# Optimization experiments

Measured on AMD Instinct MI355X. Metric: run time of the kernel, lower is better.

The kernel has to match this reference:

```python
import jax, jax.numpy as jnp
import numpy as np

B, C, CI, H, W = 4, 128, 64, 64, 64


def conv1x1(x, w, b):
    # x: [B,C,H,W], w: [Cout,Cin], b: [Cout]
    return jnp.einsum('bchw,oc->bohw', x, w) + b[None, :, None, None]


def setup_inputs() -> dict:
    key = jax.random.key(0)
    ks = jax.random.split(key, 10)
    s = 0.05  # keep logits in a sane range for softmax
    return {
        'x0': jax.random.normal(ks[0], (B, C, H, W), jnp.float32),
        'x1': jax.random.normal(ks[1], (B, C, H, W), jnp.float32),
        'g_w': jax.random.normal(ks[2], (CI, C), jnp.float32) * s,
        'g_b': jax.random.normal(ks[3], (CI,), jnp.float32) * s,
        'theta_w': jax.random.normal(ks[4], (CI, C), jnp.float32) * s,
        'theta_b': jax.random.normal(ks[5], (CI,), jnp.float32) * s,
        'phi_w': jax.random.normal(ks[6], (CI, C), jnp.float32) * s,
        'phi_b': jax.random.normal(ks[7], (CI,), jnp.float32) * s,
        'W_w': jax.random.normal(ks[8], (C, CI), jnp.float32) * s,
        'W_b': jax.random.normal(ks[9], (C,), jnp.float32) * s,
    }


def reference(x0, x1, g_w, g_b, theta_w, theta_b, phi_w, phi_b, W_w, W_b):
    b, c, h, w = x0.shape
    n = h * w
    ci = g_w.shape[0]
    g_x = conv1x1(x0, g_w, g_b).reshape(b, ci, n).transpose(0, 2, 1)      # [B,N,Ci]
    theta_x = conv1x1(x1, theta_w, theta_b).reshape(b, ci, n).transpose(0, 2, 1)  # [B,N,Ci]
    phi_x = conv1x1(x0, phi_w, phi_b).reshape(b, ci, n)                    # [B,Ci,N]
    f = jnp.einsum('bqc,bck->bqk', theta_x, phi_x)                         # [B,N,N]
    f_div_C = jax.nn.softmax(f, axis=-1)
    y = jnp.einsum('bqk,bkc->bqc', f_div_C, g_x)                           # [B,N,Ci]
    y = y.transpose(0, 2, 1).reshape(b, ci, h, w)
    W_y = conv1x1(y, W_w, W_b)
    return W_y + x0
```

## Files before the change

kernel.cpp:

```cpp
#include <hip/hip_runtime.h>
#include <hip/hip_bf16.h>


typedef unsigned int   u32;
typedef unsigned short u16;
typedef __attribute__((ext_vector_type(8))) short short8;
typedef __attribute__((ext_vector_type(4))) short short4v;
typedef __attribute__((ext_vector_type(4))) float f32x4;

#define LOG2E 1.4426950408889634f
#define KSPLIT 8

__device__ __forceinline__ float b2f(u16 v) {
  union { u32 u; float f; } x; x.u = ((u32)v) << 16; return x.f;
}
__device__ __forceinline__ u16 f2b(float f) {
  u32 u = __float_as_uint(f);
  return (u16)((u + 0x8000u) >> 16);
}
__device__ __forceinline__ short8 load_w_frag(const float* p, float s) {
  const float4 f0 = ((const float4*)p)[0];
  const float4 f1 = ((const float4*)p)[1];
  union { u32 w[4]; short8 s8; } r;
  r.w[0] = (u32)f2b(f0.x * s) | ((u32)f2b(f0.y * s) << 16);
  r.w[1] = (u32)f2b(f0.z * s) | ((u32)f2b(f0.w * s) << 16);
  r.w[2] = (u32)f2b(f1.x * s) | ((u32)f2b(f1.y * s) << 16);
  r.w[3] = (u32)f2b(f1.z * s) | ((u32)f2b(f1.w * s) << 16);
  return r.s8;
}


__global__ __launch_bounds__(256) void qkv_fused_kernel(
    const float* __restrict__ x0, const float* __restrict__ x1,
    const float* __restrict__ tw, const float* __restrict__ tb,
    const float* __restrict__ pw, const float* __restrict__ pb,
    const float* __restrict__ gw, const float* __restrict__ gb,
    u16* __restrict__ Q, u16* __restrict__ K, u16* __restrict__ Vt)
{
  const int n0 = blockIdx.x * 64;
  const int b  = blockIdx.y;
  const int t  = threadIdx.x;

  __shared__ __align__(16) short xt[2][64][136];

  #pragma unroll 8
  for (int i = 0; i < 64; ++i) {
    const int idx = i * 256 + t;
    const int tensor = idx >> 13;
    const int c = (idx >> 6) & 127;
    const int n = idx & 63;
    const float v = (tensor ? x1 : x0)[((size_t)b * 128 + c) * 4096 + n0 + n];
    xt[tensor][n][c] = (short)f2b(v);
  }
  asm volatile("" ::: "memory");
  __syncthreads();

  const int wave = t >> 6;
  const int lane = t & 63;
  const int quad = lane >> 4, l15 = lane & 15;

  if (wave < 2) {
    const int conv = wave;
    const float* wsrc = conv ? pw : tw;
    const float  ws   = conv ? 1.f : LOG2E;
    const short* xl   = &xt[conv ? 0 : 1][0][0];

    f32x4 acc[4][4];
    #pragma unroll
    for (int i = 0; i < 4; ++i)
      #pragma unroll
      for (int j = 0; j < 4; ++j) acc[i][j] = (f32x4){0.f, 0.f, 0.f, 0.f};

    #pragma unroll
    for (int kk = 0; kk < 4; ++kk) {
      short8 wf[4], xf[4];
      #pragma unroll
      for (int ot = 0; ot < 4; ++ot)
        wf[ot] = load_w_frag(wsrc + (ot * 16 + l15) * 128 + kk * 32 + quad * 8, ws);
      #pragma unroll
      for (int nt = 0; nt < 4; ++nt)
        xf[nt] = *(const short8*)(xl + (nt * 16 + l15) * 136 + kk * 32 + quad * 8);
      #pragma unroll
      for (int i = 0; i < 4; ++i)
        #pragma unroll
        for (int j = 0; j < 4; ++j)
          acc[i][j] = __builtin_amdgcn_mfma_f32_16x16x32_bf16(xf[i], wf[j], acc[i][j], 0, 0, 0);
    }

    u16* dst = (conv ? K : Q) + (size_t)b * 4096 * 64;
    const float* bias = conv ? pb : tb;
    const float bscale = conv ? 1.f : LOG2E;
    #pragma unroll
    for (int ot = 0; ot < 4; ++ot) {
      const float bv = bias[ot * 16 + l15] * bscale;
      #pragma unroll
      for (int nt = 0; nt < 4; ++nt)
        #pragma unroll
        for (int r = 0; r < 4; ++r) {
          const int n = n0 + nt * 16 + quad * 4 + r;
          dst[(size_t)n * 64 + ot * 16 + l15] = f2b(acc[nt][ot][r] + bv);
        }
    }
  } else {
    const int oh = wave - 2;
    const short* xl = &xt[0][0][0];

    f32x4 acc[2][4];
    #pragma unroll
    for (int i = 0; i < 2; ++i)
      #pragma unroll
      for (int j = 0; j < 4; ++j) acc[i][j] = (f32x4){0.f, 0.f, 0.f, 0.f};

    #pragma unroll
    for (int kk = 0; kk < 4; ++kk) {
      short8 wf[2], xf[4];
      #pragma unroll
      for (int ot = 0; ot < 2; ++ot)
        wf[ot] = load_w_frag(gw + ((oh * 2 + ot) * 16 + l15) * 128 + kk * 32 + quad * 8, 1.f);
      #pragma unroll
      for (int nt = 0; nt < 4; ++nt)
        xf[nt] = *(const short8*)(xl + (nt * 16 + l15) * 136 + kk * 32 + quad * 8);
      #pragma unroll
      for (int i = 0; i < 2; ++i)
        #pragma unroll
        for (int j = 0; j < 4; ++j)
          acc[i][j] = __builtin_amdgcn_mfma_f32_16x16x32_bf16(wf[i], xf[j], acc[i][j], 0, 0, 0);
    }

    u16* dst = Vt + (size_t)b * 64 * 4096;
    #pragma unroll
    for (int ot = 0; ot < 2; ++ot)
      #pragma unroll
      for (int r = 0; r < 4; ++r) {
        const int o = (oh * 2 + ot) * 16 + quad * 4 + r;
        const float bv = gb[o];
        #pragma unroll
        for (int nc = 0; nc < 4; ++nc)
          dst[(size_t)o * 4096 + n0 + nc * 16 + l15] = f2b(acc[ot][nc][r] + bv);
      }
  }
}

__global__ __launch_bounds__(256) void attn_kernel(
    const u16* __restrict__ Q, const u16* __restrict__ K,
    const u16* __restrict__ Vt, u16* __restrict__ Opart,
    float* __restrict__ Lp)
{
  const int qt = blockIdx.x, b = blockIdx.y, ks = blockIdx.z;
  const int tid  = threadIdx.x;
  const int wave = tid >> 6;
  const int lane = tid & 63;
  const int quad = lane >> 4;
  const int l15  = lane & 15;

  __shared__ __align__(16) short P_lds[4][64][72];
  short* pw = &P_lds[wave][0][0];

  const int q0 = qt * 256 + wave * 64;
  const u16* Qb = Q  + (size_t)b * 4096 * 64;
  const u16* Kb = K  + (size_t)b * 4096 * 64;
  const u16* Vb = Vt + (size_t)b * 64 * 4096;

  short8 qf[4][2];
  #pragma unroll
  for (int nt = 0; nt < 4; ++nt) {
    const u16* qp = Qb + (size_t)(q0 + nt * 16 + l15) * 64 + quad * 8;
    qf[nt][0] = *(const short8*)qp;
    qf[nt][1] = *(const short8*)(qp + 32);
  }

  f32x4 oacc[4][4];
  #pragma unroll
  for (int i = 0; i < 4; ++i)
    #pragma unroll
    for (int j = 0; j < 4; ++j)
      oacc[i][j] = (f32x4){0.f, 0.f, 0.f, 0.f};
  float lsum[4] = {0.f, 0.f, 0.f, 0.f};

  const int kbase = ks * (4096 / KSPLIT);
  const int NKT   = 4096 / KSPLIT / 64;

  short8 kf[4][2];
  #pragma unroll
  for (int mt = 0; mt < 4; ++mt) {
    const u16* kp = Kb + (size_t)(kbase + mt * 16 + l15) * 64 + quad * 8;
    kf[mt][0] = *(const short8*)kp;
    kf[mt][1] = *(const short8*)(kp + 32);
  }

  for (int kt = 0; kt < NKT; ++kt) {
    const int k0 = kbase + kt * 64;

    short8 vf[4][2];
    #pragma unroll
    for (int nd = 0; nd < 4; ++nd) {
      const u16* vp = Vb + (size_t)(nd * 16 + l15) * 4096 + k0 + quad * 8;
      vf[nd][0] = *(const short8*)vp;
      vf[nd][1] = *(const short8*)(vp + 32);
    }

    #pragma unroll
    for (int mt = 0; mt < 4; ++mt) {
      #pragma unroll
      for (int nt = 0; nt < 4; ++nt) {
        f32x4 s = {0.f, 0.f, 0.f, 0.f};
        s = __builtin_amdgcn_mfma_f32_16x16x32_bf16(kf[mt][0], qf[nt][0], s, 0, 0, 0);
        s = __builtin_amdgcn_mfma_f32_16x16x32_bf16(kf[mt][1], qf[nt][1], s, 0, 0, 0);
        float p0 = exp2f(s[0]), p1 = exp2f(s[1]), p2 = exp2f(s[2]), p3 = exp2f(s[3]);
        lsum[nt] += (p0 + p1) + (p2 + p3);
        u32 u0 = __float_as_uint(p0) + 0x8000u;
        u32 u1 = __float_as_uint(p1) + 0x8000u;
        u32 u2 = __float_as_uint(p2) + 0x8000u;
        u32 u3 = __float_as_uint(p3) + 0x8000u;
        union { uint2 u; short4v s4; } pk;
        pk.u.x = __builtin_amdgcn_perm(u1, u0, 0x07060302u);
        pk.u.y = __builtin_amdgcn_perm(u3, u2, 0x07060302u);
        *(short4v*)(pw + (nt * 16 + l15) * 72 + mt * 16 + quad * 4) = pk.s4;
      }
    }

    if (kt < NKT - 1) {
      #pragma unroll
      for (int mt = 0; mt < 4; ++mt) {
        const u16* kp = Kb + (size_t)(k0 + 64 + mt * 16 + l15) * 64 + quad * 8;
        kf[mt][0] = *(const short8*)kp;
        kf[mt][1] = *(const short8*)(kp + 32);
      }
    }

    asm volatile("" ::: "memory");

    #pragma unroll
    for (int mq = 0; mq < 4; ++mq) {
      const short* pr = pw + (mq * 16 + l15) * 72 + quad * 8;
      short8 pa0 = *(const short8*)pr;
      short8 pa1 = *(const short8*)(pr + 32);
      #pragma unroll
      for (int nd = 0; nd < 4; ++nd) {
        oacc[mq][nd] = __builtin_amdgcn_mfma_f32_16x16x32_bf16(pa0, vf[nd][0], oacc[mq][nd], 0, 0, 0);
        oacc[mq][nd] = __builtin_amdgcn_mfma_f32_16x16x32_bf16(pa1, vf[nd][1], oacc[mq][nd], 0, 0, 0);
      }
    }

    asm volatile("" ::: "memory");
  }

  #pragma unroll
  for (int nt = 0; nt < 4; ++nt) {
    float v = lsum[nt];
    v += __shfl_xor(v, 16, 64);
    v += __shfl_xor(v, 32, 64);
    lsum[nt] = v;
  }
  float* LpB = Lp + ((size_t)ks * 4 + b) * 4096;
  if (quad == 0) {
    #pragma unroll
    for (int nt = 0; nt < 4; ++nt)
      LpB[q0 + nt * 16 + l15] = lsum[nt];
  }

  u16* Ob = Opart + ((size_t)ks * 4 + b) * 4096 * 64;
  #pragma unroll
  for (int mq = 0; mq < 4; ++mq)
    #pragma unroll
    for (int nd = 0; nd < 4; ++nd)
      #pragma unroll
      for (int r = 0; r < 4; ++r) {
        int q = q0 + mq * 16 + quad * 4 + r;
        Ob[(size_t)q * 64 + nd * 16 + l15] = f2b(oacc[mq][nd][r]);
      }
}

__global__ __launch_bounds__(256) void out_fused_kernel(
    const u16* __restrict__ Opart, const float* __restrict__ Lp,
    const float* __restrict__ Wf, const float* __restrict__ Wbf,
    const float* __restrict__ x0, float* __restrict__ out)
{
  const int n0 = blockIdx.x * 64;
  const int b  = blockIdx.y;
  const int t  = threadIdx.x;

  __shared__ __align__(16) short Ys[64][72];

  {
    const int nl = t >> 2;
    const int q4 = t & 3;
    const int ng = n0 + nl;

    float l = 0.f;
    #pragma unroll
    for (int ks = 0; ks < KSPLIT; ++ks)
      l += Lp[((size_t)ks * 4 + b) * 4096 + ng];

    float a[16];
    #pragma unroll
    for (int j = 0; j < 16; ++j) a[j] = 0.f;
    #pragma unroll
    for (int ks = 0; ks < KSPLIT; ++ks) {
      const uint4* row = (const uint4*)(Opart + (((size_t)ks * 4 + b) * 4096 + ng) * 64 + q4 * 16);
      #pragma unroll
      for (int v = 0; v < 2; ++v) {
        uint4 r = row[v];
        u32 wds[4] = {r.x, r.y, r.z, r.w};
        #pragma unroll
        for (int j = 0; j < 4; ++j) {
          a[v * 8 + 2 * j]     += __uint_as_float(wds[j] << 16);
          a[v * 8 + 2 * j + 1] += __uint_as_float(wds[j] & 0xffff0000u);
        }
      }
    }
    const float rinv = 1.f / l;
    union { u32 w[8]; short8 s8[2]; } pk;
    #pragma unroll
    for (int j = 0; j < 8; ++j)
      pk.w[j] = (u32)f2b(a[2 * j] * rinv) | ((u32)f2b(a[2 * j + 1] * rinv) << 16);
    *(short8*)&Ys[nl][q4 * 16]     = pk.s8[0];
    *(short8*)&Ys[nl][q4 * 16 + 8] = pk.s8[1];
  }
  asm volatile("" ::: "memory");
  __syncthreads();

  const int wave = t >> 6;
  const int lane = t & 63;
  const int quad = lane >> 4, l15 = lane & 15;

  f32x4 acc[2][4];
  #pragma unroll
  for (int i = 0; i < 2; ++i)
    #pragma unroll
    for (int j = 0; j < 4; ++j) acc[i][j] = (f32x4){0.f, 0.f, 0.f, 0.f};

  #pragma unroll
  for (int kk = 0; kk < 2; ++kk) {
    short8 wf[2], yf[4];
    #pragma unroll
    for (int ot = 0; ot < 2; ++ot)
      wf[ot] = load_w_frag(Wf + ((wave * 2 + ot) * 16 + l15) * 64 + kk * 32 + quad * 8, 1.f);
    #pragma unroll
    for (int nt = 0; nt < 4; ++nt)
      yf[nt] = *(const short8*)&Ys[nt * 16 + l15][kk * 32 + quad * 8];
    #pragma unroll
    for (int i = 0; i < 2; ++i)
      #pragma unroll
      for (int j = 0; j < 4; ++j)
        acc[i][j] = __builtin_amdgcn_mfma_f32_16x16x32_bf16(wf[i], yf[j], acc[i][j], 0, 0, 0);
  }

  #pragma unroll
  for (int ot = 0; ot < 2; ++ot)
    #pragma unroll
    for (int r = 0; r < 4; ++r) {
      const int o = (wave * 2 + ot) * 16 + quad * 4 + r;
      const float bv = Wbf[o];
      #pragma unroll
      for (int nt = 0; nt < 4; ++nt) {
        const size_t idx = ((size_t)(b * 128 + o)) * 4096 + n0 + nt * 16 + l15;
        out[idx] = acc[ot][nt][r] + bv + x0[idx];
      }
    }
}

extern "C" void kernel_launch(void* const* d_in, const int* in_sizes, int n_in,
                              void* d_out, int out_size, void* d_ws, size_t ws_size,
                              hipStream_t stream) {
  const float* x0 = (const float*)d_in[0];
  const float* x1 = (const float*)d_in[1];
  const float* gw = (const float*)d_in[2];
  const float* gb = (const float*)d_in[3];
  const float* tw = (const float*)d_in[4];
  const float* tb = (const float*)d_in[5];
  const float* pw = (const float*)d_in[6];
  const float* pb = (const float*)d_in[7];
  const float* Ww = (const float*)d_in[8];
  const float* Wb = (const float*)d_in[9];
  float* out = (float*)d_out;

  char* ws = (char*)d_ws;
  u16*   Qw    = (u16*)(ws + 0);
  u16*   Kw    = (u16*)(ws + (2u << 20));
  u16*   Vtw   = (u16*)(ws + (4u << 20));
  u16*   Opart = (u16*)(ws + (6u << 20));
  float* Lp    = (float*)(ws + (22u << 20));

  qkv_fused_kernel<<<dim3(64, 4), dim3(256), 0, stream>>>(
      x0, x1, tw, tb, pw, pb, gw, gb, Qw, Kw, Vtw);

  attn_kernel<<<dim3(16, 4, KSPLIT), dim3(256), 0, stream>>>(Qw, Kw, Vtw, Opart, Lp);

  out_fused_kernel<<<dim3(64, 4), dim3(256), 0, stream>>>(
      Opart, Lp, Ww, Wb, x0, out);
}
```

Before: 137.3 us.

## Stage K/V tiles in double-buffered LDS shared across waves; vectorize input transpose

The attention kernel now loads each 64-key K tile and V tile once per block into double-buffered shared memory with coalesced 16-byte loads, prefetching the next tile into registers while the current one is computed. Previously each of the four waves fetched the same K/V fragments from global memory on its own. This cuts redundant global/L2 traffic by up to 4x, at the cost of extra LDS, two block-wide barriers per iteration, and possibly lower occupancy. The QKV kernel's input transpose also switches to float4 loads with scattered 2-byte LDS stores.

Result: faster. 133.5 us (-2.8%).

```diff
diff --git a/kernel.cpp b/kernel.cpp
--- a/kernel.cpp
+++ b/kernel.cpp
@@ -43,14 +43,19 @@
 
   __shared__ __align__(16) short xt[2][64][136];
 
-  #pragma unroll 8
-  for (int i = 0; i < 64; ++i) {
+  #pragma unroll
+  for (int i = 0; i < 16; ++i) {
     const int idx = i * 256 + t;
-    const int tensor = idx >> 13;
-    const int c = (idx >> 6) & 127;
-    const int n = idx & 63;
-    const float v = (tensor ? x1 : x0)[((size_t)b * 128 + c) * 4096 + n0 + n];
-    xt[tensor][n][c] = (short)f2b(v);
+    const int tensor = idx >> 11;
+    const int c  = (idx >> 4) & 127;
+    const int n4 = idx & 15;
+    const float4 v = *(const float4*)(
+        (tensor ? x1 : x0) + ((size_t)b * 128 + c) * 4096 + n0 + n4 * 4);
+    short* d = &xt[tensor][n4 * 4][c];
+    d[0]       = (short)f2b(v.x);
+    d[136]     = (short)f2b(v.y);
+    d[2 * 136] = (short)f2b(v.z);
+    d[3 * 136] = (short)f2b(v.w);
   }
   asm volatile("" ::: "memory");
   __syncthreads();
@@ -153,6 +158,8 @@
   const int quad = lane >> 4;
   const int l15  = lane & 15;
 
+  __shared__ __align__(16) short K_lds[2][64][72];
+  __shared__ __align__(16) short V_lds[2][64][72];
   __shared__ __align__(16) short P_lds[4][64][72];
   short* pw = &P_lds[wave][0][0];
 
@@ -161,6 +168,12 @@
   const u16* Kb = K  + (size_t)b * 4096 * 64;
   const u16* Vb = Vt + (size_t)b * 64 * 4096;
 
+  const int kbase = ks * (4096 / KSPLIT);
+  const int NKT   = 4096 / KSPLIT / 64;
+
+  const int r0 = tid >> 3;
+  const int c0 = tid & 7;
+
   short8 qf[4][2];
   #pragma unroll
   for (int nt = 0; nt < 4; ++nt) {
@@ -177,26 +190,38 @@
       oacc[i][j] = (f32x4){0.f, 0.f, 0.f, 0.f};
   float lsum[4] = {0.f, 0.f, 0.f, 0.f};
 
-  const int kbase = ks * (4096 / KSPLIT);
-  const int NKT   = 4096 / KSPLIT / 64;
-
-  short8 kf[4][2];
-  #pragma unroll
-  for (int mt = 0; mt < 4; ++mt) {
-    const u16* kp = Kb + (size_t)(kbase + mt * 16 + l15) * 64 + quad * 8;
-    kf[mt][0] = *(const short8*)kp;
-    kf[mt][1] = *(const short8*)(kp + 32);
-  }
+  {
+    const u16* kg = Kb + (size_t)kbase * 64;
+    uint4 ka0 = *(const uint4*)(kg + (size_t)r0 * 64 + c0 * 8);
+    uint4 ka1 = *(const uint4*)(kg + (size_t)(r0 + 32) * 64 + c0 * 8);
+    uint4 va0 = *(const uint4*)(Vb + (size_t)r0 * 4096 + kbase + c0 * 8);
+    uint4 va1 = *(const uint4*)(Vb + (size_t)(r0 + 32) * 4096 + kbase + c0 * 8);
+    *(uint4*)&K_lds[0][r0][c0 * 8]      = ka0;
+    *(uint4*)&K_lds[0][r0 + 32][c0 * 8] = ka1;
+    *(uint4*)&V_lds[0][r0][c0 * 8]      = va0;
+    *(uint4*)&V_lds[0][r0 + 32][c0 * 8] = va1;
+  }
+  __syncthreads();
 
   for (int kt = 0; kt < NKT; ++kt) {
-    const int k0 = kbase + kt * 64;
-
-    short8 vf[4][2];
-    #pragma unroll
-    for (int nd = 0; nd < 4; ++nd) {
-      const u16* vp = Vb + (size_t)(nd * 16 + l15) * 4096 + k0 + quad * 8;
-      vf[nd][0] = *(const short8*)vp;
-      vf[nd][1] = *(const short8*)(vp + 32);
+    const int buf = kt & 1;
+    const bool pre = (kt + 1 < NKT);
+
+    uint4 ka0, ka1, va0, va1;
+    if (pre) {
+      const int k1 = kbase + (kt + 1) * 64;
+      const u16* kg = Kb + (size_t)k1 * 64;
+      ka0 = *(const uint4*)(kg + (size_t)r0 * 64 + c0 * 8);
+      ka1 = *(const uint4*)(kg + (size_t)(r0 + 32) * 64 + c0 * 8);
+      va0 = *(const uint4*)(Vb + (size_t)r0 * 4096 + k1 + c0 * 8);
+      va1 = *(const uint4*)(Vb + (size_t)(r0 + 32) * 4096 + k1 + c0 * 8);
+    }
+
+    short8 kf[4][2];
+    #pragma unroll
+    for (int mt = 0; mt < 4; ++mt) {
+      kf[mt][0] = *(const short8*)&K_lds[buf][mt * 16 + l15][quad * 8];
+      kf[mt][1] = *(const short8*)&K_lds[buf][mt * 16 + l15][quad * 8 + 32];
     }
 
     #pragma unroll
@@ -219,16 +244,14 @@
       }
     }
 
-    if (kt < NKT - 1) {
-      #pragma unroll
-      for (int mt = 0; mt < 4; ++mt) {
-        const u16* kp = Kb + (size_t)(k0 + 64 + mt * 16 + l15) * 64 + quad * 8;
-        kf[mt][0] = *(const short8*)kp;
-        kf[mt][1] = *(const short8*)(kp + 32);
-      }
-    }
-
     asm volatile("" ::: "memory");
+
+    short8 vf[4][2];
+    #pragma unroll
+    for (int nd = 0; nd < 4; ++nd) {
+      vf[nd][0] = *(const short8*)&V_lds[buf][nd * 16 + l15][quad * 8];
+      vf[nd][1] = *(const short8*)&V_lds[buf][nd * 16 + l15][quad * 8 + 32];
+    }
 
     #pragma unroll
     for (int mq = 0; mq < 4; ++mq) {
@@ -243,6 +266,16 @@
     }
 
     asm volatile("" ::: "memory");
+
+    __syncthreads();
+    if (pre) {
+      const int nb = buf ^ 1;
+      *(uint4*)&K_lds[nb][r0][c0 * 8]      = ka0;
+      *(uint4*)&K_lds[nb][r0 + 32][c0 * 8] = ka1;
+      *(uint4*)&V_lds[nb][r0][c0 * 8]      = va0;
+      *(uint4*)&V_lds[nb][r0 + 32][c0 * 8] = va1;
+      __syncthreads();
+    }
   }
 
   #pragma unroll
```
